# Kernel tuning notes

Measured on AMD Instinct MI355X. Metric: run time of the kernel, lower is better.

The kernel has to match this reference:

```python
import jax, jax.numpy as jnp
import numpy as np

N_HEADS = 6
N_POINTS = 4
EPS = 1e-6


def layer_norm(x, g, b):
    m = jnp.mean(x, axis=-1, keepdims=True)
    v = jnp.var(x, axis=-1, keepdims=True)
    return (x - m) * jax.lax.rsqrt(v + EPS) * g + b


def bilinear_sample(value_l, h, w, loc):
    """value_l: (B, h*w, H, Dh); loc: (B, Lq, H, P, 2) normalized to [0,1].
    grid_sample semantics: align_corners=False, padding_mode='zeros'.
    Returns (B, H, Lq, P, Dh)."""
    B, HW, Hh, Dh = value_l.shape
    Lq, P = loc.shape[1], loc.shape[3]
    v = jnp.transpose(value_l, (0, 2, 1, 3))  # (B,H,HW,Dh)
    x = loc[..., 0] * w - 0.5
    y = loc[..., 1] * h - 0.5
    x0 = jnp.floor(x)
    y0 = jnp.floor(y)
    wx = x - x0
    wy = y - y0

    def gather(xi, yi):
        valid = (xi >= 0) & (xi < w) & (yi >= 0) & (yi < h)
        xc = jnp.clip(xi, 0, w - 1).astype(jnp.int32)
        yc = jnp.clip(yi, 0, h - 1).astype(jnp.int32)
        idx = yc * w + xc  # (B,Lq,H,P)
        idx_t = jnp.transpose(idx, (0, 2, 1, 3)).reshape(B, Hh, Lq * P)
        g = jnp.take_along_axis(v, idx_t[..., None], axis=2)  # (B,H,Lq*P,Dh)
        g = g.reshape(B, Hh, Lq, P, Dh)
        m = jnp.transpose(valid, (0, 2, 1, 3))[..., None].astype(g.dtype)
        return g * m

    g00 = gather(x0, y0)
    g01 = gather(x0 + 1, y0)
    g10 = gather(x0, y0 + 1)
    g11 = gather(x0 + 1, y0 + 1)
    wx_t = jnp.transpose(wx, (0, 2, 1, 3))[..., None]
    wy_t = jnp.transpose(wy, (0, 2, 1, 3))[..., None]
    top = g00 * (1 - wx_t) + g01 * wx_t
    bot = g10 * (1 - wx_t) + g11 * wx_t
    return top * (1 - wy_t) + bot * wy_t


def ms_deform_attn(qn, ref, feat_n, Wv, bv, Woff, boff, Waw, baw, Wout, bout, shapes, starts):
    B, Lq, C = qn.shape
    Hh, P, Lv = N_HEADS, N_POINTS, len(shapes)
    Dh = C // Hh
    value = (feat_n @ Wv + bv).reshape(B, -1, Hh, Dh)
    off = (qn @ Woff + boff).reshape(B, Lq, Hh, Lv, P, 2)
    aw = (qn @ Waw + baw).reshape(B, Lq, Hh, Lv * P)
    aw = jax.nn.softmax(aw, axis=-1).reshape(B, Lq, Hh, Lv, P)
    # offset normalizer is [W, H] per level
    normalizer = jnp.asarray([[w_, h_] for (h_, w_) in shapes], dtype=qn.dtype)
    loc = ref[:, :, None, :, None, :] + off / normalizer[None, None, None, :, None, :]
    out = 0.0
    for l, (h_, w_) in enumerate(shapes):
        value_l = jax.lax.dynamic_slice_in_dim(value, starts[l], h_ * w_, axis=1)
        sampled = bilinear_sample(value_l, h_, w_, loc[:, :, :, l])  # (B,H,Lq,P,Dh)
        out = out + jnp.einsum('bhqpd,bqhp->bqhd', sampled, aw[:, :, :, l])
    out = out.reshape(B, Lq, C)
    return out @ Wout + bout


def setup_inputs() -> dict:
    key = jax.random.key(0)
    ks = jax.random.split(key, 12)
    B, Lq, C, M = 2, 4096, 384, 4
    H, P, Lv = N_HEADS, N_POINTS, 1
    s = 0.02
    inp = {}
    inp['query'] = jax.random.normal(ks[0], (B, Lq, C), jnp.float32)
    inp['reference_points'] = jax.random.uniform(ks[1], (B, Lq, Lv, 2), jnp.float32)
    inp['feat'] = jax.random.normal(ks[2], (B, Lq, C), jnp.float32)
    inp['feat_other'] = jax.random.normal(ks[3], (M - 1, B, Lq, C), jnp.float32)
    inp['qn_g'] = jnp.ones((C,), jnp.float32)
    inp['qn_b'] = jnp.zeros((C,), jnp.float32)
    inp['fn_g'] = jnp.ones((M, C), jnp.float32)
    inp['fn_b'] = jnp.zeros((M, C), jnp.float32)
    inp['Wv'] = jax.random.normal(ks[4], (M, C, C), jnp.float32) * s
    inp['bv'] = jnp.zeros((M, C), jnp.float32)
    inp['Woff'] = jax.random.normal(ks[5], (M, C, H * Lv * P * 2), jnp.float32) * s
    inp['boff'] = jax.random.normal(ks[6], (M, H * Lv * P * 2), jnp.float32) * 0.5
    inp['Waw'] = jax.random.normal(ks[7], (M, C, H * Lv * P), jnp.float32) * s
    inp['baw'] = jnp.zeros((M, H * Lv * P), jnp.float32)
    inp['Wout'] = jax.random.normal(ks[8], (M, C, C), jnp.float32) * s
    inp['bout'] = jnp.zeros((M, C), jnp.float32)
    inp['gamma'] = jax.random.normal(ks[9], (M, C), jnp.float32) * 0.1
    inp['spatial_shapes'] = np.array([[64, 64]], dtype=np.int64)
    inp['level_start_index'] = np.array([0], dtype=np.int64)
    return inp


def reference(query, reference_points, feat, feat_other, qn_g, qn_b, fn_g, fn_b,
              Wv, bv, Woff, boff, Waw, baw, Wout, bout, gamma,
              spatial_shapes, level_start_index):
    shapes = [(int(h), int(w)) for h, w in np.asarray(spatial_shapes)]
    starts = [int(v) for v in np.asarray(level_start_index)]
    qn = layer_norm(query, qn_g, qn_b)
    feats = [feat] + [feat_other[i] for i in range(feat_other.shape[0])]
    out = query
    for m in range(len(feats)):
        fn = layer_norm(feats[m], fn_g[m], fn_b[m])
        attn = ms_deform_attn(qn, reference_points, fn,
                              Wv[m], bv[m], Woff[m], boff[m],
                              Waw[m], baw[m], Wout[m], bout[m], shapes, starts)
        out = out + gamma[m] * attn
    return out
```

## Files before the change

kernel.cpp:

```cpp
#include <hip/hip_runtime.h>
#include <hip/hip_bf16.h>

#define RTOT 8192
#define C_   384
#define M_   4
#define KOUT 1536

typedef __bf16 bf16;
typedef bf16  bf16x8 __attribute__((ext_vector_type(8)));
typedef float f32x4  __attribute__((ext_vector_type(4)));

#define GLOAD_LDS16(g, l) __builtin_amdgcn_global_load_lds( \
    (const __attribute__((address_space(1))) unsigned int*)(g), \
    (__attribute__((address_space(3))) unsigned int*)(l), 16, 0, 0)

#define WAITB(N) do { \
    asm volatile("s_waitcnt vmcnt(" #N ")\n\ts_barrier" ::: "memory"); \
    __builtin_amdgcn_sched_barrier(0); } while (0)

#define S0 589824
#define S1 786432
#define S2 1376256
#define S3 1376768
#define S4 1377152

__global__ __launch_bounds__(256) void cvt_kernel(
    const float* __restrict__ Wv, const float* __restrict__ Woff,
    const float* __restrict__ Waw, const float* __restrict__ Wout,
    const float* __restrict__ gamma, const float* __restrict__ boff,
    const float* __restrict__ baw, const float* __restrict__ bout,
    bf16* __restrict__ WvT, bf16* __restrict__ WoffawT, bf16* __restrict__ WoutT,
    float* __restrict__ oabias, float* __restrict__ boutbig)
{
    for (int idx = blockIdx.x * 256 + threadIdx.x; idx < S4; idx += gridDim.x * 256) {
        if (idx < S0) {
            int t = idx; int m = t / (C_ * C_); int rr = t % (C_ * C_);
            int n = rr / C_, k = rr % C_;
            WvT[t] = (bf16)Wv[(size_t)m * C_ * C_ + (size_t)k * C_ + n];
        } else if (idx < S1) {
            int t = idx - S0; int m = t / (128 * C_); int rr = t % (128 * C_);
            int n = rr / C_, k = rr % C_;
            float v = 0.f;
            if (n < 48)      v = Woff[(size_t)m * C_ * 48 + (size_t)k * 48 + n];
            else if (n < 72) v = Waw[(size_t)m * C_ * 24 + (size_t)k * 24 + (n - 48)];
            WoffawT[t] = (bf16)v;
        } else if (idx < S2) {
            int t = idx - S1; int n = t / KOUT; int kk = t % KOUT;
            int m = kk / C_, k = kk % C_;
            WoutT[t] = (bf16)(Wout[(size_t)m * C_ * C_ + (size_t)k * C_ + n] * gamma[m * C_ + n]);
        } else if (idx < S3) {
            int t = idx - S2; int m = t / 128; int n = t % 128;
            float v = 0.f;
            if (n < 48)      v = boff[m * 48 + n];
            else if (n < 72) v = baw[m * 24 + (n - 48)];
            oabias[t] = v;
        } else {
            int c = idx - S3;
            float s = 0.f;
            for (int m = 0; m < M_; ++m) s += gamma[m * C_ + c] * bout[m * C_ + c];
            boutbig[c] = s;
        }
    }
}

__global__ __launch_bounds__(256) void ln_kernel(
    const float* __restrict__ query, const float* __restrict__ feat,
    const float* __restrict__ feat_other,
    const float* __restrict__ qn_g, const float* __restrict__ qn_b,
    const float* __restrict__ fn_g, const float* __restrict__ fn_b,
    bf16* __restrict__ qn, bf16* __restrict__ fn)
{
    const int r = blockIdx.x * 4 + (threadIdx.x >> 6);
    const int which = blockIdx.y;
    const int lane = threadIdx.x & 63;
    const float* src; const float* g; const float* bb; bf16* dst;
    if (which == 0) { src = query; g = qn_g; bb = qn_b; dst = qn; }
    else {
        int m = which - 1;
        src = (m == 0) ? feat : feat_other + (size_t)(m - 1) * RTOT * C_;
        g = fn_g + m * C_; bb = fn_b + m * C_; dst = fn + (size_t)m * RTOT * C_;
    }
    src += (size_t)r * C_; dst += (size_t)r * C_;
    float v[6]; float s = 0.f, sq = 0.f;
#pragma unroll
    for (int j = 0; j < 6; ++j) {
        v[j] = src[lane + j * 64];
        s += v[j]; sq += v[j] * v[j];
    }
#pragma unroll
    for (int o = 1; o < 64; o <<= 1) {
        s += __shfl_xor(s, o);
        sq += __shfl_xor(sq, o);
    }
    const float mean = s * (1.f / C_);
    const float var  = sq * (1.f / C_) - mean * mean;
    const float rs   = rsqrtf(var + 1e-6f);
#pragma unroll
    for (int j = 0; j < 6; ++j) {
        int c = lane + j * 64;
        dst[c] = (bf16)((v[j] - mean) * rs * g[c] + bb[c]);
    }
}

__device__ __forceinline__ void gemm_pipe(
    const bf16* __restrict__ A, int lda,
    const bf16* __restrict__ W, int ldw,
    const float* __restrict__ bias,
    void* __restrict__ outP, int ldo, int mode,
    int brow, int bcol, bf16* As, bf16* Bs)
{
    const int tid = threadIdx.x;
    const int lane = tid & 63, wave = tid >> 6;
    const int wr = wave >> 1, wc = wave & 1;
    const int lr = lane & 15, lg = lane >> 4;

    const int r0 = tid >> 2, s0 = tid & 3;
    const int r1 = r0 + 64;
    const long long aoff0 = (long long)(brow + r0) * lda + (s0 ^ ((r0 >> 1) & 3)) * 8;
    const long long aoff1 = (long long)(brow + r1) * lda + (s0 ^ ((r1 >> 1) & 3)) * 8;
    const long long woff0 = (long long)(bcol + r0) * ldw + (s0 ^ ((r0 >> 1) & 3)) * 8;
    const long long woff1 = (long long)(bcol + r1) * ldw + (s0 ^ ((r1 >> 1) & 3)) * 8;

    int aRd[4], bRd[4];
#pragma unroll
    for (int i = 0; i < 4; ++i) {
        const int ra = wr * 64 + i * 16 + lr;
        const int rb = wc * 64 + i * 16 + lr;
        aRd[i] = ra * 32 + (lg ^ ((ra >> 1) & 3)) * 8;
        bRd[i] = rb * 32 + (lg ^ ((rb >> 1) & 3)) * 8;
    }

    f32x4 acc[4][4] = {};

#pragma unroll
    for (int t = 0; t < 2; ++t) {
        GLOAD_LDS16(A + aoff0 + t * 32, (char*)As + t * 8192 + tid * 16);
        GLOAD_LDS16(A + aoff1 + t * 32, (char*)As + t * 8192 + (tid + 256) * 16);
        GLOAD_LDS16(W + woff0 + t * 32, (char*)Bs + t * 8192 + tid * 16);
        GLOAD_LDS16(W + woff1 + t * 32, (char*)Bs + t * 8192 + (tid + 256) * 16);
    }

#pragma unroll
    for (int kt = 0; kt < 12; ++kt) {
        if (kt + 1 < 12) { WAITB(4); } else { WAITB(0); }
        const int cb = kt % 3, ib = (kt + 2) % 3;
        if (kt + 2 < 12) {
            GLOAD_LDS16(A + aoff0 + (kt + 2) * 32, (char*)As + ib * 8192 + tid * 16);
            GLOAD_LDS16(A + aoff1 + (kt + 2) * 32, (char*)As + ib * 8192 + (tid + 256) * 16);
            GLOAD_LDS16(W + woff0 + (kt + 2) * 32, (char*)Bs + ib * 8192 + tid * 16);
            GLOAD_LDS16(W + woff1 + (kt + 2) * 32, (char*)Bs + ib * 8192 + (tid + 256) * 16);
        }
        bf16x8 af[4], bfr[4];
#pragma unroll
        for (int mi = 0; mi < 4; ++mi)
            af[mi] = *reinterpret_cast<const bf16x8*>(&As[cb * 4096 + aRd[mi]]);
#pragma unroll
        for (int ni = 0; ni < 4; ++ni)
            bfr[ni] = *reinterpret_cast<const bf16x8*>(&Bs[cb * 4096 + bRd[ni]]);
#pragma unroll
        for (int mi = 0; mi < 4; ++mi)
#pragma unroll
            for (int ni = 0; ni < 4; ++ni)
                acc[mi][ni] = __builtin_amdgcn_mfma_f32_16x16x32_bf16(
                    af[mi], bfr[ni], acc[mi][ni], 0, 0, 0);
    }

#pragma unroll
    for (int mi = 0; mi < 4; ++mi) {
#pragma unroll
        for (int ni = 0; ni < 4; ++ni) {
#pragma unroll
            for (int rr = 0; rr < 4; ++rr) {
                const int row = brow + wr * 64 + mi * 16 + lg * 4 + rr;
                const int col = bcol + wc * 64 + ni * 16 + lr;
                float v = acc[mi][ni][rr];
                if (mode != 3) v += bias[col];
                const long long o = (long long)row * ldo + col;
                if (mode == 1) ((float*)outP)[o] = v;
                else           ((bf16*)outP)[o] = (bf16)v;
            }
        }
    }
}

__global__ __launch_bounds__(256) void g01_kernel(
    const bf16* __restrict__ fn, const bf16* __restrict__ qn,
    const bf16* __restrict__ WvT, const bf16* __restrict__ WoffawT,
    const float* __restrict__ bv, const float* __restrict__ oabias,
    bf16* __restrict__ value, float* __restrict__ offaw)
{
    __shared__ __align__(16) bf16 As[3 * 4096];
    __shared__ __align__(16) bf16 Bs[3 * 4096];
    const int id = blockIdx.x;
    if (id < 768) {
        const int rowb = id & 63, q = id >> 6;
        const int colb = q % 3, m = q / 3;
        gemm_pipe(fn + (long long)m * RTOT * C_, C_,
                  WvT + (long long)m * C_ * C_, C_,
                  bv + m * C_, value + (long long)m * RTOT * C_, C_, 0,
                  rowb * 128, colb * 128, As, Bs);
    } else {
        const int id2 = id - 768;
        const int rowb = id2 & 63, m = id2 >> 6;
        gemm_pipe(qn, C_, WoffawT + (long long)m * 128 * C_, C_,
                  oabias + m * 128, offaw + (long long)m * RTOT * 128, 128, 1,
                  rowb * 128, 0, As, Bs);
    }
}

__global__ __launch_bounds__(256) void g2_kernel(
    const bf16* __restrict__ attn, const bf16* __restrict__ WoutT,
    bf16* __restrict__ partial)
{
    __shared__ __align__(16) bf16 As[3 * 4096];
    __shared__ __align__(16) bf16 Bs[3 * 4096];
    const int rowb = blockIdx.x & 63;
    const int q = blockIdx.x >> 6;
    const int colb = q % 3, kc = q / 3;
    gemm_pipe(attn + kc * C_, KOUT, WoutT + kc * C_, KOUT, nullptr,
              partial + (long long)kc * RTOT * C_, C_, 3,
              rowb * 128, colb * 128, As, Bs);
}

__global__ __launch_bounds__(256) void combine_kernel(
    const bf16* __restrict__ partial, const float* __restrict__ query,
    const float* __restrict__ boutbig, float* __restrict__ out)
{
    const int i8 = (blockIdx.x * 256 + threadIdx.x) * 8;
    const int c0 = i8 % C_;
    float s[8];
#pragma unroll
    for (int j = 0; j < 8; ++j) s[j] = query[i8 + j] + boutbig[c0 + j];
#pragma unroll
    for (int z = 0; z < 4; ++z) {
        bf16x8 p = *reinterpret_cast<const bf16x8*>(partial + (long long)z * RTOT * C_ + i8);
#pragma unroll
        for (int j = 0; j < 8; ++j) s[j] += (float)p[j];
    }
#pragma unroll
    for (int j = 0; j < 8; ++j) out[i8 + j] = s[j];
}

struct WP { float w; int off; };

__global__ __launch_bounds__(384) void sample_kernel(
    const float* __restrict__ offaw, const float* __restrict__ ref,
    const bf16* __restrict__ value, bf16* __restrict__ attn)
{
    const int bid   = blockIdx.x;
    const int combo = bid & 7;
    const int pair  = bid >> 3;
    const int m = combo >> 1, b = combo & 1;
    const int r0 = b * 4096 + pair * 2;

    __shared__ WP wp_s[2][24][4];

    const int t = threadIdx.x;
    if (t < 48) {
        const int row = t / 24;
        const int i   = t % 24;
        const int h = i >> 2, p = i & 3;
        const int r = r0 + row;
        const float* oa = offaw + ((long long)m * RTOT + r) * 128;
        float e = oa[48 + h * 4 + p];
        float mx = fmaxf(e, __shfl_xor(e, 1));
        mx = fmaxf(mx, __shfl_xor(mx, 2));
        float ex = expf(e - mx);
        float s = ex;
        s += __shfl_xor(s, 1);
        s += __shfl_xor(s, 2);
        const float aw = ex / s;
        const float x = ref[r * 2 + 0] * 64.f - 0.5f + oa[h * 8 + p * 2 + 0];
        const float y = ref[r * 2 + 1] * 64.f - 0.5f + oa[h * 8 + p * 2 + 1];
        const float xf = floorf(x), yf = floorf(y);
        const float wx = x - xf, wy = y - yf;
        const int x0 = (int)xf, y0 = (int)yf;
        const bool xok0 = (x0 >= 0) && (x0 < 64);
        const bool xok1 = (x0 >= -1) && (x0 < 63);
        const bool yok0 = (y0 >= 0) && (y0 < 64);
        const bool yok1 = (y0 >= -1) && (y0 < 63);
        const int xc0 = min(max(x0, 0), 63),     xc1 = min(max(x0 + 1, 0), 63);
        const int yc0 = min(max(y0, 0), 63),     yc1 = min(max(y0 + 1, 0), 63);
        WP w0 = { aw * (1.f - wx) * (1.f - wy) * (float)(xok0 && yok0), (yc0 * 64 + xc0) * (C_ * 2) };
        WP w1 = { aw * wx         * (1.f - wy) * (float)(xok1 && yok0), (yc0 * 64 + xc1) * (C_ * 2) };
        WP w2 = { aw * (1.f - wx) * wy         * (float)(xok0 && yok1), (yc1 * 64 + xc0) * (C_ * 2) };
        WP w3 = { aw * wx         * wy         * (float)(xok1 && yok1), (yc1 * 64 + xc1) * (C_ * 2) };
        wp_s[row][i][0] = w0;  wp_s[row][i][1] = w1;
        wp_s[row][i][2] = w2;  wp_s[row][i][3] = w3;
    }
    __syncthreads();

    const int row = t / 192;
    const int tl  = t % 192;
    const int h   = tl >> 5;
    const int l32 = tl & 31;
    const int r   = r0 + row;
    const char* vb = (const char*)(value
        + ((long long)m * RTOT + (long long)b * 4096) * C_ + h * 64 + l32 * 2);

    float wreg[16]; int oreg[16]; unsigned int vreg[16];
#pragma unroll
    for (int i = 0; i < 16; ++i) {
        WP wp = wp_s[row][h * 4 + (i >> 2)][i & 3];
        wreg[i] = wp.w; oreg[i] = wp.off;
    }
#pragma unroll
    for (int i = 0; i < 16; ++i)
        vreg[i] = *reinterpret_cast<const unsigned int*>(vb + oreg[i]);
    float acc0 = 0.f, acc1 = 0.f;
#pragma unroll
    for (int i = 0; i < 16; ++i) {
        unsigned int u = vreg[i];
        float lo = __builtin_bit_cast(float, u << 16);
        float hi = __builtin_bit_cast(float, u & 0xffff0000u);
        acc0 += wreg[i] * lo;
        acc1 += wreg[i] * hi;
    }
    union { bf16 h2[2]; unsigned int u; } o;
    o.h2[0] = (bf16)acc0; o.h2[1] = (bf16)acc1;
    *reinterpret_cast<unsigned int*>(attn + (long long)r * KOUT + m * C_ + h * 64 + l32 * 2) = o.u;
}

extern "C" void kernel_launch(void* const* d_in, const int* in_sizes, int n_in,
                              void* d_out, int out_size, void* d_ws, size_t ws_size,
                              hipStream_t stream)
{
    const float* query      = (const float*)d_in[0];
    const float* ref        = (const float*)d_in[1];
    const float* feat       = (const float*)d_in[2];
    const float* feat_other = (const float*)d_in[3];
    const float* qn_g = (const float*)d_in[4];
    const float* qn_b = (const float*)d_in[5];
    const float* fn_g = (const float*)d_in[6];
    const float* fn_b = (const float*)d_in[7];
    const float* Wv   = (const float*)d_in[8];
    const float* bv   = (const float*)d_in[9];
    const float* Woff = (const float*)d_in[10];
    const float* boff = (const float*)d_in[11];
    const float* Waw  = (const float*)d_in[12];
    const float* baw  = (const float*)d_in[13];
    const float* Wout = (const float*)d_in[14];
    const float* bout = (const float*)d_in[15];
    const float* gamma = (const float*)d_in[16];
    float* out = (float*)d_out;

    char* ws = (char*)d_ws;
    size_t off = 0;
    auto carve = [&](size_t bytes) { char* p = ws + off; off += (bytes + 255) & ~(size_t)255; return p; };
    bf16*  qn      = (bf16*)carve((size_t)RTOT * C_ * 2);
    bf16*  fn      = (bf16*)carve((size_t)M_ * RTOT * C_ * 2);
    bf16*  value   = (bf16*)carve((size_t)M_ * RTOT * C_ * 2);
    bf16*  attn    = (bf16*)carve((size_t)RTOT * KOUT * 2);
    bf16*  partial = (bf16*)carve((size_t)M_ * RTOT * C_ * 2);
    float* offaw   = (float*)carve((size_t)M_ * RTOT * 128 * 4);
    bf16*  WvT     = (bf16*)carve((size_t)M_ * C_ * C_ * 2);
    bf16*  WoffawT = (bf16*)carve((size_t)M_ * 128 * C_ * 2);
    bf16*  WoutT   = (bf16*)carve((size_t)C_ * KOUT * 2);
    float* oabias  = (float*)carve((size_t)M_ * 128 * 4);
    float* boutbig = (float*)carve((size_t)C_ * 4);

    cvt_kernel<<<2048, 256, 0, stream>>>(Wv, Woff, Waw, Wout, gamma, boff, baw, bout,
                                         WvT, WoffawT, WoutT, oabias, boutbig);
    ln_kernel<<<dim3(RTOT / 4, 5), 256, 0, stream>>>(query, feat, feat_other,
                                                     qn_g, qn_b, fn_g, fn_b, qn, fn);
    g01_kernel<<<1024, 256, 0, stream>>>(fn, qn, WvT, WoffawT, bv, oabias, value, offaw);
    sample_kernel<<<dim3(RTOT * M_ / 2), 384, 0, stream>>>(offaw, ref, value, attn);
    g2_kernel<<<768, 256, 0, stream>>>(attn, WoutT, partial);
    combine_kernel<<<1536, 256, 0, stream>>>(partial, query, boutbig, out);
}
```

Measured before the change: 110.4 us.

## Merge prep kernels, fuse split-K combine into g2, widen sample loads

Merges the weight-conversion and layer-norm kernels into one launch and has the layer-norm path read float2. The combine kernel is folded into g2: the last of four split-K blocks per tile, found through an atomic counter, sums the partials and writes the output. The sample kernel now handles four rows per block and has each thread load and produce four bf16 channels at once. This removes two launches and a pass over the partials, at the cost of atomics, extra fences and a serialized tail in the last block of each tile.

```diff
diff --git a/kernel.cpp b/kernel.cpp
--- a/kernel.cpp
+++ b/kernel.cpp
@@ -23,16 +23,61 @@
 #define S2 1376256
 #define S3 1376768
 #define S4 1377152
-
-__global__ __launch_bounds__(256) void cvt_kernel(
+#define S5 1377344
+
+__global__ __launch_bounds__(256) void prep_kernel(
+    const float* __restrict__ query, const float* __restrict__ feat,
+    const float* __restrict__ feat_other,
+    const float* __restrict__ qn_g, const float* __restrict__ qn_b,
+    const float* __restrict__ fn_g, const float* __restrict__ fn_b,
+    bf16* __restrict__ qn, bf16* __restrict__ fn,
     const float* __restrict__ Wv, const float* __restrict__ Woff,
     const float* __restrict__ Waw, const float* __restrict__ Wout,
     const float* __restrict__ gamma, const float* __restrict__ boff,
     const float* __restrict__ baw, const float* __restrict__ bout,
     bf16* __restrict__ WvT, bf16* __restrict__ WoffawT, bf16* __restrict__ WoutT,
-    float* __restrict__ oabias, float* __restrict__ boutbig)
-{
-    for (int idx = blockIdx.x * 256 + threadIdx.x; idx < S4; idx += gridDim.x * 256) {
+    float* __restrict__ oabias, float* __restrict__ boutbig, int* __restrict__ counters)
+{
+    const int bid = blockIdx.x;
+    const int tid = threadIdx.x;
+    if (bid < 10240) {
+        const int which = bid / 2048;
+        const int xb    = bid % 2048;
+        const int r = xb * 4 + (tid >> 6);
+        const int lane = tid & 63;
+        const float* src; const float* g; const float* bb; bf16* dst;
+        if (which == 0) { src = query; g = qn_g; bb = qn_b; dst = qn; }
+        else {
+            int m = which - 1;
+            src = (m == 0) ? feat : feat_other + (size_t)(m - 1) * RTOT * C_;
+            g = fn_g + m * C_; bb = fn_b + m * C_; dst = fn + (size_t)m * RTOT * C_;
+        }
+        src += (size_t)r * C_; dst += (size_t)r * C_;
+        float2 v[3]; float s = 0.f, sq = 0.f;
+#pragma unroll
+        for (int j = 0; j < 3; ++j) {
+            v[j] = *reinterpret_cast<const float2*>(src + (lane + j * 64) * 2);
+            s += v[j].x + v[j].y; sq += v[j].x * v[j].x + v[j].y * v[j].y;
+        }
+#pragma unroll
+        for (int o = 1; o < 64; o <<= 1) {
+            s += __shfl_xor(s, o);
+            sq += __shfl_xor(sq, o);
+        }
+        const float mean = s * (1.f / C_);
+        const float var  = sq * (1.f / C_) - mean * mean;
+        const float rs   = rsqrtf(var + 1e-6f);
+#pragma unroll
+        for (int j = 0; j < 3; ++j) {
+            const int c = (lane + j * 64) * 2;
+            union { bf16 h2[2]; unsigned int u; } o;
+            o.h2[0] = (bf16)((v[j].x - mean) * rs * g[c] + bb[c]);
+            o.h2[1] = (bf16)((v[j].y - mean) * rs * g[c + 1] + bb[c + 1]);
+            *reinterpret_cast<unsigned int*>(dst + c) = o.u;
+        }
+        return;
+    }
+    for (int idx = (bid - 10240) * 256 + tid; idx < S5; idx += 1024 * 256) {
         if (idx < S0) {
             int t = idx; int m = t / (C_ * C_); int rr = t % (C_ * C_);
             int n = rr / C_, k = rr % C_;
@@ -54,51 +99,14 @@
             if (n < 48)      v = boff[m * 48 + n];
             else if (n < 72) v = baw[m * 24 + (n - 48)];
             oabias[t] = v;
-        } else {
+        } else if (idx < S4) {
             int c = idx - S3;
             float s = 0.f;
             for (int m = 0; m < M_; ++m) s += gamma[m * C_ + c] * bout[m * C_ + c];
             boutbig[c] = s;
-        }
-    }
-}
-
-__global__ __launch_bounds__(256) void ln_kernel(
-    const float* __restrict__ query, const float* __restrict__ feat,
-    const float* __restrict__ feat_other,
-    const float* __restrict__ qn_g, const float* __restrict__ qn_b,
-    const float* __restrict__ fn_g, const float* __restrict__ fn_b,
-    bf16* __restrict__ qn, bf16* __restrict__ fn)
-{
-    const int r = blockIdx.x * 4 + (threadIdx.x >> 6);
-    const int which = blockIdx.y;
-    const int lane = threadIdx.x & 63;
-    const float* src; const float* g; const float* bb; bf16* dst;
-    if (which == 0) { src = query; g = qn_g; bb = qn_b; dst = qn; }
-    else {
-        int m = which - 1;
-        src = (m == 0) ? feat : feat_other + (size_t)(m - 1) * RTOT * C_;
-        g = fn_g + m * C_; bb = fn_b + m * C_; dst = fn + (size_t)m * RTOT * C_;
-    }
-    src += (size_t)r * C_; dst += (size_t)r * C_;
-    float v[6]; float s = 0.f, sq = 0.f;
-#pragma unroll
-    for (int j = 0; j < 6; ++j) {
-        v[j] = src[lane + j * 64];
-        s += v[j]; sq += v[j] * v[j];
-    }
-#pragma unroll
-    for (int o = 1; o < 64; o <<= 1) {
-        s += __shfl_xor(s, o);
-        sq += __shfl_xor(sq, o);
-    }
-    const float mean = s * (1.f / C_);
-    const float var  = sq * (1.f / C_) - mean * mean;
-    const float rs   = rsqrtf(var + 1e-6f);
-#pragma unroll
-    for (int j = 0; j < 6; ++j) {
-        int c = lane + j * 64;
-        dst[c] = (bf16)((v[j] - mean) * rs * g[c] + bb[c]);
+        } else {
+            counters[idx - S4] = 0;
+        }
     }
 }
 
@@ -210,35 +218,44 @@
 
 __global__ __launch_bounds__(256) void g2_kernel(
     const bf16* __restrict__ attn, const bf16* __restrict__ WoutT,
-    bf16* __restrict__ partial)
+    bf16* __restrict__ partial, const float* __restrict__ query,
+    const float* __restrict__ boutbig, float* __restrict__ out,
+    int* __restrict__ counters)
 {
     __shared__ __align__(16) bf16 As[3 * 4096];
     __shared__ __align__(16) bf16 Bs[3 * 4096];
-    const int rowb = blockIdx.x & 63;
-    const int q = blockIdx.x >> 6;
-    const int colb = q % 3, kc = q / 3;
+    const int tile = blockIdx.x >> 2;
+    const int kc   = blockIdx.x & 3;
+    const int rowb = tile % 64, colb = tile / 64;
     gemm_pipe(attn + kc * C_, KOUT, WoutT + kc * C_, KOUT, nullptr,
               partial + (long long)kc * RTOT * C_, C_, 3,
               rowb * 128, colb * 128, As, Bs);
-}
-
-__global__ __launch_bounds__(256) void combine_kernel(
-    const bf16* __restrict__ partial, const float* __restrict__ query,
-    const float* __restrict__ boutbig, float* __restrict__ out)
-{
-    const int i8 = (blockIdx.x * 256 + threadIdx.x) * 8;
-    const int c0 = i8 % C_;
-    float s[8];
-#pragma unroll
-    for (int j = 0; j < 8; ++j) s[j] = query[i8 + j] + boutbig[c0 + j];
-#pragma unroll
-    for (int z = 0; z < 4; ++z) {
-        bf16x8 p = *reinterpret_cast<const bf16x8*>(partial + (long long)z * RTOT * C_ + i8);
-#pragma unroll
-        for (int j = 0; j < 8; ++j) s[j] += (float)p[j];
-    }
-#pragma unroll
-    for (int j = 0; j < 8; ++j) out[i8 + j] = s[j];
+
+    __threadfence();
+    __shared__ int lastv;
+    if (threadIdx.x == 0) lastv = atomicAdd(&counters[tile], 1);
+    __syncthreads();
+    if (lastv != 3) return;
+    __threadfence();
+
+    const int row  = rowb * 128 + (threadIdx.x >> 1);
+    const int cb0  = colb * 128 + (threadIdx.x & 1) * 64;
+    const long long rb = (long long)row * C_;
+#pragma unroll
+    for (int j = 0; j < 8; ++j) {
+        const int col = cb0 + j * 8;
+        float s[8];
+#pragma unroll
+        for (int jj = 0; jj < 8; ++jj) s[jj] = query[rb + col + jj] + boutbig[col + jj];
+#pragma unroll
+        for (int z = 0; z < 4; ++z) {
+            bf16x8 p = *reinterpret_cast<const bf16x8*>(partial + (long long)z * RTOT * C_ + rb + col);
+#pragma unroll
+            for (int jj = 0; jj < 8; ++jj) s[jj] += (float)p[jj];
+        }
+#pragma unroll
+        for (int jj = 0; jj < 8; ++jj) out[rb + col + jj] = s[jj];
+    }
 }
 
 struct WP { float w; int off; };
@@ -249,14 +266,14 @@
 {
     const int bid   = blockIdx.x;
     const int combo = bid & 7;
-    const int pair  = bid >> 3;
+    const int quad  = bid >> 3;
     const int m = combo >> 1, b = combo & 1;
-    const int r0 = b * 4096 + pair * 2;
-
-    __shared__ WP wp_s[2][24][4];
+    const int r0 = b * 4096 + quad * 4;
+
+    __shared__ WP wp_s[4][24][4];
 
     const int t = threadIdx.x;
-    if (t < 48) {
+    if (t < 96) {
         const int row = t / 24;
         const int i   = t % 24;
         const int h = i >> 2, p = i & 3;
@@ -290,15 +307,15 @@
     }
     __syncthreads();
 
-    const int row = t / 192;
-    const int tl  = t % 192;
-    const int h   = tl >> 5;
-    const int l32 = tl & 31;
+    const int row = t / 96;
+    const int tl  = t % 96;
+    const int h   = tl >> 4;
+    const int l16 = tl & 15;
     const int r   = r0 + row;
     const char* vb = (const char*)(value
-        + ((long long)m * RTOT + (long long)b * 4096) * C_ + h * 64 + l32 * 2);
-
-    float wreg[16]; int oreg[16]; unsigned int vreg[16];
+        + ((long long)m * RTOT + (long long)b * 4096) * C_ + h * 64 + l16 * 4);
+
+    float wreg[16]; int oreg[16]; unsigned long long vreg[16];
 #pragma unroll
     for (int i = 0; i < 16; ++i) {
         WP wp = wp_s[row][h * 4 + (i >> 2)][i & 3];
@@ -306,19 +323,20 @@
     }
 #pragma unroll
     for (int i = 0; i < 16; ++i)
-        vreg[i] = *reinterpret_cast<const unsigned int*>(vb + oreg[i]);
-    float acc0 = 0.f, acc1 = 0.f;
+        vreg[i] = *reinterpret_cast<const unsigned long long*>(vb + oreg[i]);
+    float a0 = 0.f, a1 = 0.f, a2 = 0.f, a3 = 0.f;
 #pragma unroll
     for (int i = 0; i < 16; ++i) {
-        unsigned int u = vreg[i];
-        float lo = __builtin_bit_cast(float, u << 16);
-        float hi = __builtin_bit_cast(float, u & 0xffff0000u);
-        acc0 += wreg[i] * lo;
-        acc1 += wreg[i] * hi;
-    }
-    union { bf16 h2[2]; unsigned int u; } o;
-    o.h2[0] = (bf16)acc0; o.h2[1] = (bf16)acc1;
-    *reinterpret_cast<unsigned int*>(attn + (long long)r * KOUT + m * C_ + h * 64 + l32 * 2) = o.u;
+        const unsigned int lo = (unsigned int)vreg[i];
+        const unsigned int hi = (unsigned int)(vreg[i] >> 32);
+        a0 += wreg[i] * __builtin_bit_cast(float, lo << 16);
+        a1 += wreg[i] * __builtin_bit_cast(float, lo & 0xffff0000u);
+        a2 += wreg[i] * __builtin_bit_cast(float, hi << 16);
+        a3 += wreg[i] * __builtin_bit_cast(float, hi & 0xffff0000u);
+    }
+    union { bf16 h4[4]; unsigned long long u; } o;
+    o.h4[0] = (bf16)a0; o.h4[1] = (bf16)a1; o.h4[2] = (bf16)a2; o.h4[3] = (bf16)a3;
+    *reinterpret_cast<unsigned long long*>(attn + (long long)r * KOUT + m * C_ + h * 64 + l16 * 4) = o.u;
 }
 
 extern "C" void kernel_launch(void* const* d_in, const int* in_sizes, int n_in,
@@ -358,13 +376,13 @@
     bf16*  WoutT   = (bf16*)carve((size_t)C_ * KOUT * 2);
     float* oabias  = (float*)carve((size_t)M_ * 128 * 4);
     float* boutbig = (float*)carve((size_t)C_ * 4);
-
-    cvt_kernel<<<2048, 256, 0, stream>>>(Wv, Woff, Waw, Wout, gamma, boff, baw, bout,
-                                         WvT, WoffawT, WoutT, oabias, boutbig);
-    ln_kernel<<<dim3(RTOT / 4, 5), 256, 0, stream>>>(query, feat, feat_other,
-                                                     qn_g, qn_b, fn_g, fn_b, qn, fn);
+    int*   counters = (int*)carve(192 * 4);
+
+    prep_kernel<<<11264, 256, 0, stream>>>(query, feat, feat_other,
+                                           qn_g, qn_b, fn_g, fn_b, qn, fn,
+                                           Wv, Woff, Waw, Wout, gamma, boff, baw, bout,
+                                           WvT, WoffawT, WoutT, oabias, boutbig, counters);
     g01_kernel<<<1024, 256, 0, stream>>>(fn, qn, WvT, WoffawT, bv, oabias, value, offaw);
-    sample_kernel<<<dim3(RTOT * M_ / 2), 384, 0, stream>>>(offaw, ref, value, attn);
-    g2_kernel<<<768, 256, 0, stream>>>(attn, WoutT, partial);
-    combine_kernel<<<1536, 256, 0, stream>>>(partial, query, boutbig, out);
-}
+    sample_kernel<<<dim3(RTOT * M_ / 4), 384, 0, stream>>>(offaw, ref, value, attn);
+    g2_kernel<<<768, 256, 0, stream>>>(attn, WoutT, partial, query, boutbig, out, counters);
+}
```

Result: slower. 288.8 us (+161.6%).
